# Optimization experiments

Hardware: AMD Instinct MI355X
Metric: run time of the kernel (lower is better)

Reference implementation:

```python
import jax, jax.numpy as jnp
import numpy as np

B, N, T, CIN, COUT, K, DIL = 8, 207, 12, 64, 64, 3, 1


def setup_inputs() -> dict:
    key = jax.random.key(0)
    ks = jax.random.split(key, 13)
    s = 0.05
    return {
        "X": jax.random.normal(ks[0], (B, N, T, CIN), jnp.float32),
        "wA": jax.random.normal(ks[1], (COUT, CIN, 1, K), jnp.float32) * s,
        "bA": jax.random.normal(ks[2], (COUT,), jnp.float32) * s,
        "wB": jax.random.normal(ks[3], (COUT, CIN, 1, K), jnp.float32) * s,
        "bB": jax.random.normal(ks[4], (COUT,), jnp.float32) * s,
        "wq": jax.random.normal(ks[5], (COUT // 8, COUT), jnp.float32) * s,
        "bq": jax.random.normal(ks[6], (COUT // 8,), jnp.float32) * s,
        "wk": jax.random.normal(ks[7], (COUT // 8, COUT), jnp.float32) * s,
        "bk": jax.random.normal(ks[8], (COUT // 8,), jnp.float32) * s,
        "wv": jax.random.normal(ks[9], (COUT, COUT), jnp.float32) * s,
        "bv": jax.random.normal(ks[10], (COUT,), jnp.float32) * s,
        "gamma": jax.random.normal(ks[11], (1,), jnp.float32) * 0.1,
    }


def reference(X, wA, bA, wB, bB, wq, bq, wk, bk, wv, bv, gamma):
    # X: [B, N, T, C] -> [B, C, N, T]
    x = jnp.transpose(X, (0, 3, 1, 2))
    k_size = wA.shape[-1]
    pad = (k_size - 1) * DIL  # causal left pad == pad-both + drop-right in torch code

    def causal_conv(w, b):
        y = jax.lax.conv_general_dilated(
            x, w, window_strides=(1, 1),
            padding=((0, 0), (pad, 0)),
            rhs_dilation=(1, DIL),
            dimension_numbers=("NCHW", "OIHW", "NCHW"))
        return y + b[None, :, None, None]

    A = causal_conv(wA, bA)
    Bg = causal_conv(wB, bB)
    h = A * jax.nn.sigmoid(Bg)  # [B, C, N, T]

    b_, c, w_, h_ = h.shape
    L = w_ * h_
    h2 = h.reshape(b_, c, L)  # [B, C, L]
    q = jnp.einsum("oc,bcl->bol", wq, h2) + bq[None, :, None]  # [B, C/8, L]
    kk = jnp.einsum("oc,bcl->bol", wk, h2) + bk[None, :, None]
    v = jnp.einsum("oc,bcl->bol", wv, h2) + bv[None, :, None]   # [B, C, L]

    energy = jnp.einsum("bql,bqm->blm", q, kk)  # [B, L, L]
    attn = jax.nn.softmax(energy, axis=-1)
    out = jnp.einsum("bcm,blm->bcl", v, attn).reshape(b_, c, w_, h_)
    out = gamma[0] * out + h
    return jnp.transpose(out, (0, 2, 3, 1))  # [B, N, T, C]
```

## Files before the change

kernel.cpp:

```cpp
#include <hip/hip_runtime.h>
#include <hip/hip_bf16.h>

#define Bn 8
#define Nn 207
#define Tn 12
#define Cn 64
#define Ln (Nn*Tn)
#define LP 2496
#define NT 39
#define NB 104

typedef unsigned int u32;
typedef unsigned short u16;
typedef _Float16 f16;
typedef __attribute__((ext_vector_type(4))) _Float16 half4;
typedef __attribute__((ext_vector_type(4))) float floatx4;

__device__ __forceinline__ u16 f2h(float f) { f16 h = (f16)f; return *(u16*)&h; }
__device__ __forceinline__ float h2f_lo(u32 u) { u16 x = (u16)u;        f16 h = *(f16*)&x; return (float)h; }
__device__ __forceinline__ float h2f_hi(u32 u) { u16 x = (u16)(u >> 16); f16 h = *(f16*)&x; return (float)h; }

#define W_PW   0
#define U_WVT  24576
#define F_WK   14336
#define F_WQ   14848
#define U_K    30720
#define U_Q    190464
#define U_HT   350208

__global__ __launch_bounds__(256) void prep_kernel(
    const float* __restrict__ wA, const float* __restrict__ wB,
    const float* __restrict__ wq, const float* __restrict__ wk,
    const float* __restrict__ wv, float* __restrict__ ws)
{
    u16* wsu = (u16*)ws;
    u32* wsw = (u32*)ws;
    int idx = blockIdx.x * 256 + threadIdx.x;
    if (idx < 12288) {
        int co = idx & 63, j = (idx >> 6) & 7, cig = (idx >> 9) & 7, k = idx >> 12;
        int src = (co*64 + cig*8 + j)*3 + k;
        wsw[W_PW + idx] = (u32)f2h(wA[src]) | ((u32)f2h(wB[src]) << 16);
    } else if (idx < 16384) {
        int j = idx - 12288;
        wsu[U_WVT + j] = f2h(wv[j]);
    } else if (idx < 16896) {
        int j = idx - 16384; int o = j & 7, c = j >> 3;
        ws[F_WK + j] = wk[o*Cn + c];
    } else if (idx < 17408) {
        int j = idx - 16896; int o = j & 7, c = j >> 3;
        ws[F_WQ + j] = wq[o*Cn + c];
    } else if (idx < 18944) {
        int j = idx - 17408;
        int b = j / 192, rem = j - b*192;
        int which = rem / 96, rr = rem - which*96;
        wsu[(which ? U_Q : U_K) + (size_t)b*LP*8 + Ln*8 + rr] = 0;
    } else if (idx < 25088) {
        int j = idx - 18944;
        int b = j / 768, rem = j - b*768;
        int c = rem / 12, mm = 52 + (rem - c*12);
        int ss = mm >> 4, q = (mm >> 2) & 3, i = mm & 3;
        int cs = c >> 4, rm = c & 15;
        wsu[U_HT + (size_t)b*NT*4096 + ((38*16 + ss*4 + cs)*256 + (rm*4 + q)*4 + i)] = 0;
    }
}

__global__ __launch_bounds__(256, 2) void conv_k_kernel(
    const float* __restrict__ X,
    const float* __restrict__ bA, const float* __restrict__ bB,
    const float* __restrict__ bk, const float* __restrict__ bq,
    float* __restrict__ ws, float* __restrict__ out)
{
    __shared__ u32   w_s[12288];
    __shared__ float xs[Tn*Cn];
    __shared__ float hs[Tn*Cn];
    __shared__ float wkq_s[1024];
    int b = blockIdx.x & 7;
    int n = blockIdx.x >> 3;
    int tid = threadIdx.x;

    for (int i = tid; i < 3072; i += 256)
        ((uint4*)w_s)[i] = ((const uint4*)ws)[i];
    const float* Xp = X + (size_t)(b*Nn + n)*Tn*Cn;
    for (int i = tid; i < (Tn*Cn)/4; i += 256)
        ((float4*)xs)[i] = ((const float4*)Xp)[i];
    ((float4*)wkq_s)[tid] = ((const float4*)(ws + F_WK))[tid];
    __syncthreads();

    int co = tid & 63;
    int tg = tid >> 6;
    float aA[3] = {bA[co], bA[co], bA[co]};
    float aB[3] = {bB[co], bB[co], bB[co]};
    int tb = tg*3 - 2;

    #pragma unroll 1
    for (int cig = 0; cig < 8; ++cig) {
        float xr[5][8];
        #pragma unroll
        for (int d = 0; d < 5; ++d) {
            int tp = tb + d;
            if (tp >= 0) {
                float4 xa = *(const float4*)(xs + tp*Cn + cig*8);
                float4 xb = *(const float4*)(xs + tp*Cn + cig*8 + 4);
                xr[d][0]=xa.x; xr[d][1]=xa.y; xr[d][2]=xa.z; xr[d][3]=xa.w;
                xr[d][4]=xb.x; xr[d][5]=xb.y; xr[d][6]=xb.z; xr[d][7]=xb.w;
            } else {
                #pragma unroll
                for (int j = 0; j < 8; ++j) xr[d][j] = 0.f;
            }
        }
        #pragma unroll
        for (int k = 0; k < 3; ++k) {
            #pragma unroll
            for (int j = 0; j < 8; ++j) {
                u32 p = w_s[((k*8 + cig)*8 + j)*64 + co];
                float wa = h2f_lo(p), wb = h2f_hi(p);
                #pragma unroll
                for (int tt = 0; tt < 3; ++tt) {
                    aA[tt] += xr[tt + k][j] * wa;
                    aB[tt] += xr[tt + k][j] * wb;
                }
            }
        }
    }

    #pragma unroll
    for (int tt = 0; tt < 3; ++tt) {
        int t = tg*3 + tt;
        float hv = aA[tt] * (1.f / (1.f + __expf(-aB[tt])));
        hs[t*Cn + co] = hv;
        out[((size_t)b*Ln + (size_t)n*Tn + t)*Cn + co] = hv;
    }
    __syncthreads();

    if (tid < 96) {
        int r = tid >> 3, o = tid & 7;
        float acc = bk[o];
        for (int c = 0; c < Cn; ++c) acc += hs[r*Cn + c] * wkq_s[c*8 + o];
        ((u16*)ws)[U_K + (size_t)b*LP*8 + ((size_t)n*Tn + r)*8 + o] = f2h(acc);
    } else if (tid < 192) {
        int r = (tid - 96) >> 3, o = tid & 7;
        float acc = bq[o];
        for (int c = 0; c < Cn; ++c) acc += hs[r*Cn + c] * wkq_s[512 + c*8 + o];
        ((u16*)ws)[U_Q + (size_t)b*LP*8 + ((size_t)n*Tn + r)*8 + o] = f2h(acc);
    }
    {
        int jj = tid >> 6, c = tid & 63;
        if (jj < 3) {
            int m = n*Tn + 4*jj;
            int tile = m >> 6, mloc = m & 63;
            int ss = mloc >> 4, q = (mloc >> 2) & 3;
            int cs = c >> 4, rm = c & 15;
            u32 p0 = ((u32)f2h(hs[(4*jj+1)*Cn + c]) << 16) | f2h(hs[(4*jj+0)*Cn + c]);
            u32 p1 = ((u32)f2h(hs[(4*jj+3)*Cn + c]) << 16) | f2h(hs[(4*jj+2)*Cn + c]);
            u16* ht = (u16*)ws + U_HT + (size_t)b*NT*4096
                    + ((tile*16 + ss*4 + cs)*256 + (rm*4 + q)*4);
            *(uint2*)ht = make_uint2(p0, p1);
        }
    }
}

__global__ __launch_bounds__(256, 3) void attn_kernel(
    const float* __restrict__ gamma, const float* __restrict__ bv,
    const float* __restrict__ ws, float* __restrict__ out)
{
    __shared__ float part[4*64*24];
    __shared__ float den_part[4][32];

    int b  = blockIdx.x & 7;
    int nb = blockIdx.x >> 3;
    int R0 = nb*24;
    int tid = threadIdx.x;
    int lane = tid & 63;
    int w = tid >> 6;
    int rm = lane & 15;
    int quad = lane >> 4;

    const u16* wsu = (const u16*)ws;
    const u16* kb = wsu + U_K  + (size_t)b*LP*8;
    const u16* qb = wsu + U_Q  + (size_t)b*LP*8;
    const u16* hb = wsu + U_HT + (size_t)b*NT*4096;

    half4 qf0, qf1;
    {
        uint2 u0 = make_uint2(0, 0), u1 = make_uint2(0, 0);
        int r0 = R0 + rm;       if (r0 >= LP) r0 = LP - 1;
        int r1 = R0 + 16 + rm;  if (r1 >= LP) r1 = LP - 1;
        if (quad < 2) {
            u0 = *(const uint2*)(qb + (size_t)r0*8 + 4*quad);
            u1 = *(const uint2*)(qb + (size_t)r1*8 + 4*quad);
        }
        qf0 = *(half4*)&u0; qf1 = *(half4*)&u1;
    }

    floatx4 acc[4][2];
    #pragma unroll
    for (int cs = 0; cs < 4; ++cs)
        #pragma unroll
        for (int g = 0; g < 2; ++g) acc[cs][g] = (floatx4){0.f, 0.f, 0.f, 0.f};
    float dsum0 = 0.f, dsum1 = 0.f;

    uint2 k0_0,k0_1,k0_2,k0_3, k1_0,k1_1,k1_2,k1_3;
    uint2 h0_0,h0_1,h0_2,h0_3,h0_4,h0_5,h0_6,h0_7,h0_8,h0_9,h0_10,h0_11,h0_12,h0_13,h0_14,h0_15;
    uint2 h1_0,h1_1,h1_2,h1_3,h1_4,h1_5,h1_6,h1_7,h1_8,h1_9,h1_10,h1_11,h1_12,h1_13,h1_14,h1_15;

#define LDK(kt, SS) ((quad < 2) ? *(const uint2*)((kt) + ((SS)*16 + rm)*8 + 4*quad) : make_uint2(0,0))
#define LDH(ht, IDX) (*(const uint2*)((ht) + (IDX)*256 + lane*4))

#define LOADT(B, T) {                                                          \
    int tc = ((T) < NT) ? (T) : (NT-1);                                        \
    const u16* kt_ = kb + (size_t)tc*512;                                      \
    const u16* ht_ = hb + (size_t)tc*4096;                                     \
    k##B##_0 = LDK(kt_, 0); k##B##_1 = LDK(kt_, 1);                            \
    k##B##_2 = LDK(kt_, 2); k##B##_3 = LDK(kt_, 3);                            \
    h##B##_0  = LDH(ht_, 0);  h##B##_1  = LDH(ht_, 1);                         \
    h##B##_2  = LDH(ht_, 2);  h##B##_3  = LDH(ht_, 3);                         \
    h##B##_4  = LDH(ht_, 4);  h##B##_5  = LDH(ht_, 5);                         \
    h##B##_6  = LDH(ht_, 6);  h##B##_7  = LDH(ht_, 7);                         \
    h##B##_8  = LDH(ht_, 8);  h##B##_9  = LDH(ht_, 9);                         \
    h##B##_10 = LDH(ht_, 10); h##B##_11 = LDH(ht_, 11);                        \
    h##B##_12 = LDH(ht_, 12); h##B##_13 = LDH(ht_, 13);                        \
    h##B##_14 = LDH(ht_, 14); h##B##_15 = LDH(ht_, 15);                        \
}

#define COMPSS(KR, HA, HB_, HC, HD, T, SS) {                                   \
    half4 kf = *(half4*)&KR;                                                   \
    floatx4 s0 = {0.f,0.f,0.f,0.f}, s1 = {0.f,0.f,0.f,0.f};                    \
    s0 = __builtin_amdgcn_mfma_f32_16x16x16f16(kf, qf0, s0, 0, 0, 0);          \
    s1 = __builtin_amdgcn_mfma_f32_16x16x16f16(kf, qf1, s1, 0, 0, 0);          \
    half4 e0, e1;                                                              \
    int mb = (T)*64 + (SS)*16 + 4*quad;                                        \
    _Pragma("unroll")                                                          \
    for (int i_ = 0; i_ < 4; ++i_) {                                           \
        float ev0 = (mb + i_ < Ln) ? __expf(s0[i_]) : 0.f;                     \
        float ev1 = (mb + i_ < Ln) ? __expf(s1[i_]) : 0.f;                     \
        dsum0 += ev0; dsum1 += ev1;                                            \
        e0[i_] = (f16)ev0; e1[i_] = (f16)ev1;                                  \
    }                                                                          \
    half4 a0_ = *(half4*)&HA, a1_ = *(half4*)&HB_, a2_ = *(half4*)&HC, a3_ = *(half4*)&HD; \
    acc[0][0] = __builtin_amdgcn_mfma_f32_16x16x16f16(a0_, e0, acc[0][0], 0, 0, 0); \
    acc[0][1] = __builtin_amdgcn_mfma_f32_16x16x16f16(a0_, e1, acc[0][1], 0, 0, 0); \
    acc[1][0] = __builtin_amdgcn_mfma_f32_16x16x16f16(a1_, e0, acc[1][0], 0, 0, 0); \
    acc[1][1] = __builtin_amdgcn_mfma_f32_16x16x16f16(a1_, e1, acc[1][1], 0, 0, 0); \
    acc[2][0] = __builtin_amdgcn_mfma_f32_16x16x16f16(a2_, e0, acc[2][0], 0, 0, 0); \
    acc[2][1] = __builtin_amdgcn_mfma_f32_16x16x16f16(a2_, e1, acc[2][1], 0, 0, 0); \
    acc[3][0] = __builtin_amdgcn_mfma_f32_16x16x16f16(a3_, e0, acc[3][0], 0, 0, 0); \
    acc[3][1] = __builtin_amdgcn_mfma_f32_16x16x16f16(a3_, e1, acc[3][1], 0, 0, 0); \
}

#define COMPT(B, T) {                                                          \
    COMPSS(k##B##_0, h##B##_0,  h##B##_1,  h##B##_2,  h##B##_3,  T, 0)         \
    COMPSS(k##B##_1, h##B##_4,  h##B##_5,  h##B##_6,  h##B##_7,  T, 1)         \
    COMPSS(k##B##_2, h##B##_8,  h##B##_9,  h##B##_10, h##B##_11, T, 2)         \
    COMPSS(k##B##_3, h##B##_12, h##B##_13, h##B##_14, h##B##_15, T, 3)         \
}

    LOADT(0, w)
    for (int i = 0; i < 5; ++i) {
        int t0 = w + 8*i;
        LOADT(1, t0 + 4)
        COMPT(0, t0)
        LOADT(0, t0 + 8)
        COMPT(1, t0 + 4)
    }
#undef LOADT
#undef COMPT
#undef COMPSS
#undef LDK
#undef LDH

    {
        float s_ = dsum0;
        s_ += __shfl_xor(s_, 16, 64);
        s_ += __shfl_xor(s_, 32, 64);
        if (quad == 0) den_part[w][rm] = s_;
        float t_ = dsum1;
        t_ += __shfl_xor(t_, 16, 64);
        t_ += __shfl_xor(t_, 32, 64);
        if (quad == 0) den_part[w][16 + rm] = t_;
    }

    float* pw = part + w*1536;
    #pragma unroll
    for (int cs = 0; cs < 4; ++cs) {
        #pragma unroll
        for (int i = 0; i < 4; ++i)
            pw[(cs*16 + quad*4 + i)*24 + rm] = acc[cs][0][i];
        if (rm < 8) {
            #pragma unroll
            for (int i = 0; i < 4; ++i)
                pw[(cs*16 + quad*4 + i)*24 + 16 + rm] = acc[cs][1][i];
        }
    }
    __syncthreads();

    for (int j = tid; j < 1536; j += 256)
        part[j] = part[j] + part[1536 + j] + part[3072 + j] + part[4608 + j];
    __syncthreads();

    int o = tid & 63, rq = tid >> 6;
    float gam = gamma[0];
    float bvo = bv[o];
    const u16* wvr = wsu + U_WVT + o*64;
    uint4 wvu[8];
    #pragma unroll
    for (int x = 0; x < 8; ++x) wvu[x] = *(const uint4*)(wvr + x*8);
    #pragma unroll
    for (int rr = 0; rr < 6; ++rr) {
        int r = rq*6 + rr;
        int row = R0 + r;
        if (row < Ln) {
            float den = den_part[0][r] + den_part[1][r] + den_part[2][r] + den_part[3][r];
            float p = 0.f;
            #pragma unroll
            for (int x = 0; x < 8; ++x) {
                const f16* hh = (const f16*)&wvu[x];
                #pragma unroll
                for (int i = 0; i < 8; ++i)
                    p += (float)hh[i] * part[(x*8 + i)*24 + r];
            }
            size_t gi = ((size_t)b*Ln + row)*64 + o;
            out[gi] = gam*(bvo + p/den) + out[gi];
        }
    }
}

extern "C" void kernel_launch(void* const* d_in, const int* in_sizes, int n_in,
                              void* d_out, int out_size, void* d_ws, size_t ws_size,
                              hipStream_t stream) {
    const float* X     = (const float*)d_in[0];
    const float* wA    = (const float*)d_in[1];
    const float* bA    = (const float*)d_in[2];
    const float* wB    = (const float*)d_in[3];
    const float* bB    = (const float*)d_in[4];
    const float* wq    = (const float*)d_in[5];
    const float* bq    = (const float*)d_in[6];
    const float* wk    = (const float*)d_in[7];
    const float* bk    = (const float*)d_in[8];
    const float* wv    = (const float*)d_in[9];
    const float* bv    = (const float*)d_in[10];
    const float* gamma = (const float*)d_in[11];
    float* out = (float*)d_out;
    float* ws  = (float*)d_ws;

    prep_kernel<<<98, 256, 0, stream>>>(wA, wB, wq, wk, wv, ws);
    conv_k_kernel<<<Bn*Nn, 256, 0, stream>>>(X, bA, bB, bk, bq, ws, out);
    attn_kernel<<<Bn*NB, 256, 0, stream>>>(gamma, bv, ws, out);
}
```

Before: 160.2 us.

## Split attention key tiles across eight waves and use exp2 with folded log2e

```diff
diff --git a/kernel.cpp b/kernel.cpp
--- a/kernel.cpp
+++ b/kernel.cpp
@@ -13,8 +13,11 @@
 typedef unsigned int u32;
 typedef unsigned short u16;
 typedef _Float16 f16;
+typedef __attribute__((ext_vector_type(2))) _Float16 half2;
 typedef __attribute__((ext_vector_type(4))) _Float16 half4;
 typedef __attribute__((ext_vector_type(4))) float floatx4;
+
+#define LOG2E 1.44269504088896f
 
 __device__ __forceinline__ u16 f2h(float f) { f16 h = (f16)f; return *(u16*)&h; }
 __device__ __forceinline__ float h2f_lo(u32 u) { u16 x = (u16)u;        f16 h = *(f16*)&x; return (float)h; }
@@ -48,7 +51,7 @@
         ws[F_WK + j] = wk[o*Cn + c];
     } else if (idx < 17408) {
         int j = idx - 16896; int o = j & 7, c = j >> 3;
-        ws[F_WQ + j] = wq[o*Cn + c];
+        ws[F_WQ + j] = wq[o*Cn + c] * LOG2E;
     } else if (idx < 18944) {
         int j = idx - 17408;
         int b = j / 192, rem = j - b*192;
@@ -139,7 +142,7 @@
         ((u16*)ws)[U_K + (size_t)b*LP*8 + ((size_t)n*Tn + r)*8 + o] = f2h(acc);
     } else if (tid < 192) {
         int r = (tid - 96) >> 3, o = tid & 7;
-        float acc = bq[o];
+        float acc = bq[o] * LOG2E;
         for (int c = 0; c < Cn; ++c) acc += hs[r*Cn + c] * wkq_s[512 + c*8 + o];
         ((u16*)ws)[U_Q + (size_t)b*LP*8 + ((size_t)n*Tn + r)*8 + o] = f2h(acc);
     }
@@ -159,12 +162,12 @@
     }
 }
 
-__global__ __launch_bounds__(256, 3) void attn_kernel(
+__global__ __launch_bounds__(512, 4) void attn_kernel(
     const float* __restrict__ gamma, const float* __restrict__ bv,
     const float* __restrict__ ws, float* __restrict__ out)
 {
-    __shared__ float part[4*64*24];
-    __shared__ float den_part[4][32];
+    __shared__ float part[8*64*24];
+    __shared__ float den_part[8][32];
 
     int b  = blockIdx.x & 7;
     int nb = blockIdx.x >> 3;
@@ -191,6 +194,8 @@
         }
         qf0 = *(half4*)&u0; qf1 = *(half4*)&u1;
     }
+
+    const half2 one2 = {(f16)1.f, (f16)1.f};
 
     floatx4 acc[4][2];
     #pragma unroll
@@ -222,20 +227,13 @@
     h##B##_14 = LDH(ht_, 14); h##B##_15 = LDH(ht_, 15);                        \
 }
 
-#define COMPSS(KR, HA, HB_, HC, HD, T, SS) {                                   \
-    half4 kf = *(half4*)&KR;                                                   \
-    floatx4 s0 = {0.f,0.f,0.f,0.f}, s1 = {0.f,0.f,0.f,0.f};                    \
-    s0 = __builtin_amdgcn_mfma_f32_16x16x16f16(kf, qf0, s0, 0, 0, 0);          \
-    s1 = __builtin_amdgcn_mfma_f32_16x16x16f16(kf, qf1, s1, 0, 0, 0);          \
-    half4 e0, e1;                                                              \
-    int mb = (T)*64 + (SS)*16 + 4*quad;                                        \
-    _Pragma("unroll")                                                          \
-    for (int i_ = 0; i_ < 4; ++i_) {                                           \
-        float ev0 = (mb + i_ < Ln) ? __expf(s0[i_]) : 0.f;                     \
-        float ev1 = (mb + i_ < Ln) ? __expf(s1[i_]) : 0.f;                     \
-        dsum0 += ev0; dsum1 += ev1;                                            \
-        e0[i_] = (f16)ev0; e1[i_] = (f16)ev1;                                  \
-    }                                                                          \
+#define PVTAIL(HA, HB_, HC, HD)                                                \
+    dsum0 = __builtin_amdgcn_fdot2(e0a, one2, dsum0, false);                   \
+    dsum0 = __builtin_amdgcn_fdot2(e0b, one2, dsum0, false);                   \
+    dsum1 = __builtin_amdgcn_fdot2(e1a, one2, dsum1, false);                   \
+    dsum1 = __builtin_amdgcn_fdot2(e1b, one2, dsum1, false);                   \
+    half4 e0 = __builtin_shufflevector(e0a, e0b, 0, 1, 2, 3);                  \
+    half4 e1 = __builtin_shufflevector(e1a, e1b, 0, 1, 2, 3);                  \
     half4 a0_ = *(half4*)&HA, a1_ = *(half4*)&HB_, a2_ = *(half4*)&HC, a3_ = *(half4*)&HD; \
     acc[0][0] = __builtin_amdgcn_mfma_f32_16x16x16f16(a0_, e0, acc[0][0], 0, 0, 0); \
     acc[0][1] = __builtin_amdgcn_mfma_f32_16x16x16f16(a0_, e1, acc[0][1], 0, 0, 0); \
@@ -244,27 +242,76 @@
     acc[2][0] = __builtin_amdgcn_mfma_f32_16x16x16f16(a2_, e0, acc[2][0], 0, 0, 0); \
     acc[2][1] = __builtin_amdgcn_mfma_f32_16x16x16f16(a2_, e1, acc[2][1], 0, 0, 0); \
     acc[3][0] = __builtin_amdgcn_mfma_f32_16x16x16f16(a3_, e0, acc[3][0], 0, 0, 0); \
-    acc[3][1] = __builtin_amdgcn_mfma_f32_16x16x16f16(a3_, e1, acc[3][1], 0, 0, 0); \
-}
-
-#define COMPT(B, T) {                                                          \
-    COMPSS(k##B##_0, h##B##_0,  h##B##_1,  h##B##_2,  h##B##_3,  T, 0)         \
-    COMPSS(k##B##_1, h##B##_4,  h##B##_5,  h##B##_6,  h##B##_7,  T, 1)         \
-    COMPSS(k##B##_2, h##B##_8,  h##B##_9,  h##B##_10, h##B##_11, T, 2)         \
-    COMPSS(k##B##_3, h##B##_12, h##B##_13, h##B##_14, h##B##_15, T, 3)         \
+    acc[3][1] = __builtin_amdgcn_mfma_f32_16x16x16f16(a3_, e1, acc[3][1], 0, 0, 0);
+
+#define COMPSS(KR, HA, HB_, HC, HD) {                                          \
+    half4 kf = *(half4*)&KR;                                                   \
+    floatx4 s0 = {0.f,0.f,0.f,0.f}, s1 = {0.f,0.f,0.f,0.f};                    \
+    s0 = __builtin_amdgcn_mfma_f32_16x16x16f16(kf, qf0, s0, 0, 0, 0);          \
+    s1 = __builtin_amdgcn_mfma_f32_16x16x16f16(kf, qf1, s1, 0, 0, 0);          \
+    half2 e0a, e0b, e1a, e1b;                                                  \
+    e0a[0] = (f16)__builtin_amdgcn_exp2f(s0[0]);                               \
+    e0a[1] = (f16)__builtin_amdgcn_exp2f(s0[1]);                               \
+    e0b[0] = (f16)__builtin_amdgcn_exp2f(s0[2]);                               \
+    e0b[1] = (f16)__builtin_amdgcn_exp2f(s0[3]);                               \
+    e1a[0] = (f16)__builtin_amdgcn_exp2f(s1[0]);                               \
+    e1a[1] = (f16)__builtin_amdgcn_exp2f(s1[1]);                               \
+    e1b[0] = (f16)__builtin_amdgcn_exp2f(s1[2]);                               \
+    e1b[1] = (f16)__builtin_amdgcn_exp2f(s1[3]);                               \
+    PVTAIL(HA, HB_, HC, HD)                                                    \
+}
+
+#define COMPSS_M(KR, HA, HB_, HC, HD, SS) {                                    \
+    half4 kf = *(half4*)&KR;                                                   \
+    floatx4 s0 = {0.f,0.f,0.f,0.f}, s1 = {0.f,0.f,0.f,0.f};                    \
+    s0 = __builtin_amdgcn_mfma_f32_16x16x16f16(kf, qf0, s0, 0, 0, 0);          \
+    s1 = __builtin_amdgcn_mfma_f32_16x16x16f16(kf, qf1, s1, 0, 0, 0);          \
+    int mb = 38*64 + (SS)*16 + 4*quad;                                         \
+    half2 e0a, e0b, e1a, e1b;                                                  \
+    e0a[0] = (f16)((mb+0 < Ln) ? __builtin_amdgcn_exp2f(s0[0]) : 0.f);         \
+    e0a[1] = (f16)((mb+1 < Ln) ? __builtin_amdgcn_exp2f(s0[1]) : 0.f);         \
+    e0b[0] = (f16)((mb+2 < Ln) ? __builtin_amdgcn_exp2f(s0[2]) : 0.f);         \
+    e0b[1] = (f16)((mb+3 < Ln) ? __builtin_amdgcn_exp2f(s0[3]) : 0.f);         \
+    e1a[0] = (f16)((mb+0 < Ln) ? __builtin_amdgcn_exp2f(s1[0]) : 0.f);         \
+    e1a[1] = (f16)((mb+1 < Ln) ? __builtin_amdgcn_exp2f(s1[1]) : 0.f);         \
+    e1b[0] = (f16)((mb+2 < Ln) ? __builtin_amdgcn_exp2f(s1[2]) : 0.f);         \
+    e1b[1] = (f16)((mb+3 < Ln) ? __builtin_amdgcn_exp2f(s1[3]) : 0.f);         \
+    PVTAIL(HA, HB_, HC, HD)                                                    \
+}
+
+#define COMPT(B) {                                                             \
+    COMPSS(k##B##_0, h##B##_0,  h##B##_1,  h##B##_2,  h##B##_3)                \
+    COMPSS(k##B##_1, h##B##_4,  h##B##_5,  h##B##_6,  h##B##_7)                \
+    COMPSS(k##B##_2, h##B##_8,  h##B##_9,  h##B##_10, h##B##_11)               \
+    COMPSS(k##B##_3, h##B##_12, h##B##_13, h##B##_14, h##B##_15)               \
+}
+
+#define COMPT_M(B) {                                                           \
+    COMPSS_M(k##B##_0, h##B##_0,  h##B##_1,  h##B##_2,  h##B##_3,  0)          \
+    COMPSS_M(k##B##_1, h##B##_4,  h##B##_5,  h##B##_6,  h##B##_7,  1)          \
+    COMPSS_M(k##B##_2, h##B##_8,  h##B##_9,  h##B##_10, h##B##_11, 2)          \
+    COMPSS_M(k##B##_3, h##B##_12, h##B##_13, h##B##_14, h##B##_15, 3)          \
 }
 
     LOADT(0, w)
-    for (int i = 0; i < 5; ++i) {
-        int t0 = w + 8*i;
-        LOADT(1, t0 + 4)
-        COMPT(0, t0)
-        LOADT(0, t0 + 8)
-        COMPT(1, t0 + 4)
+    for (int i = 0; i < 2; ++i) {
+        int t0 = w + 16*i;
+        LOADT(1, t0 + 8)
+        COMPT(0)
+        if (i == 0 || w < 7) LOADT(0, t0 + 16)
+        COMPT(1)
+    }
+    if (w < 6) {
+        COMPT(0)
+    } else if (w == 6) {
+        COMPT_M(0)
     }
 #undef LOADT
 #undef COMPT
+#undef COMPT_M
 #undef COMPSS
+#undef COMPSS_M
+#undef PVTAIL
 #undef LDK
 #undef LDH
 
@@ -293,8 +340,11 @@
     }
     __syncthreads();
 
-    for (int j = tid; j < 1536; j += 256)
-        part[j] = part[j] + part[1536 + j] + part[3072 + j] + part[4608 + j];
+    for (int j = tid; j < 1536; j += 512) {
+        float s = part[j]        + part[1536 + j] + part[3072 + j] + part[4608 + j]
+                + part[6144 + j] + part[7680 + j] + part[9216 + j] + part[10752 + j];
+        part[j] = s;
+    }
     __syncthreads();
 
     int o = tid & 63, rq = tid >> 6;
@@ -305,11 +355,12 @@
     #pragma unroll
     for (int x = 0; x < 8; ++x) wvu[x] = *(const uint4*)(wvr + x*8);
     #pragma unroll
-    for (int rr = 0; rr < 6; ++rr) {
-        int r = rq*6 + rr;
+    for (int rr = 0; rr < 3; ++rr) {
+        int r = rq*3 + rr;
         int row = R0 + r;
         if (row < Ln) {
-            float den = den_part[0][r] + den_part[1][r] + den_part[2][r] + den_part[3][r];
+            float den = den_part[0][r] + den_part[1][r] + den_part[2][r] + den_part[3][r]
+                      + den_part[4][r] + den_part[5][r] + den_part[6][r] + den_part[7][r];
             float p = 0.f;
             #pragma unroll
             for (int x = 0; x < 8; ++x) {
@@ -344,5 +395,5 @@
 
     prep_kernel<<<98, 256, 0, stream>>>(wA, wB, wq, wk, wv, ws);
     conv_k_kernel<<<Bn*Nn, 256, 0, stream>>>(X, bA, bB, bk, bq, ws, out);
-    attn_kernel<<<Bn*NB, 256, 0, stream>>>(gamma, bv, ws, out);
-}
+    attn_kernel<<<Bn*NB, 512, 0, stream>>>(gamma, bv, ws, out);
+}
```

Result: slower. 191.7 us (+19.7%).
